# Optimization experiments

Measured on AMD Instinct MI355X. Metric: run time of the kernel, lower is better.

## Reference

```python
import jax, jax.numpy as jnp
import numpy as np
import math

DIM = 4096
N_HEADS = 32
HEAD_DIM = DIM // N_HEADS  # 128
SEQLEN = 2048


def setup_inputs() -> dict:
    key = jax.random.key(0)
    ks = jax.random.split(key, 8)
    x = jax.random.normal(ks[0], (1, SEQLEN, DIM), dtype=jnp.float32)
    # freqs_cis as real view: (seqlen, head_dim//2, 2) = (cos, sin) of rotary angles
    theta = 10000.0 ** (-jnp.arange(0, HEAD_DIM, 2, dtype=jnp.float32) / HEAD_DIM)
    angles = jnp.arange(SEQLEN, dtype=jnp.float32)[:, None] * theta[None, :]
    freqs = jnp.stack([jnp.cos(angles), jnp.sin(angles)], axis=-1)  # (S, 64, 2)
    # causal additive mask (use -1e9 instead of -inf for numeric safety)
    mask = jnp.triu(jnp.full((SEQLEN, SEQLEN), -1e9, dtype=jnp.float32), k=1)[None, None]
    scale = 1.0 / math.sqrt(DIM)
    wq = jax.random.normal(ks[1], (DIM, DIM), dtype=jnp.float32) * scale
    wk = jax.random.normal(ks[2], (DIM, DIM), dtype=jnp.float32) * scale
    wv = jax.random.normal(ks[3], (DIM, DIM), dtype=jnp.float32) * scale
    wo = jax.random.normal(ks[4], (DIM, DIM), dtype=jnp.float32) * scale
    return {"x": x, "start_pos": 0, "freqs": freqs, "mask": mask,
            "wq": wq, "wk": wk, "wv": wv, "wo": wo}


def _rotary(xq, xk, freqs, seqlen, n_heads, head_dim):
    # Faithful to source: note the repo's slice(0, 2) means xq_ == xq (no pair swap).
    ll = freqs[:, :, 0:1]  # (S, hd/2, 1) cos
    rr = freqs[:, :, 1:2]  # (S, hd/2, 1) sin
    fl = jnp.concatenate([ll, ll], axis=-1).reshape(seqlen, 1, head_dim)
    fr = jnp.concatenate([-rr, rr], axis=-1).reshape(seqlen, 1, head_dim)
    xq_ = xq.reshape(seqlen, n_heads, head_dim // 2, 2).reshape(seqlen, n_heads, head_dim)  # == xq
    xk_ = xk.reshape(seqlen, n_heads, head_dim // 2, 2).reshape(seqlen, n_heads, head_dim)  # == xk
    return xq * fl + xq_ * fr, xk * fl + xk_ * fr


def reference(x, start_pos, freqs, mask, wq, wk, wv, wo):
    bsz, seqlen, dim = x.shape  # bsz == 1 (source squeezes batch)
    xs = x[0]  # (S, D) -- HE encrypt/linear/decrypt roundtrip == plain linear
    xq = xs @ wq.T
    xk = xs @ wk.T
    xv = xs @ wv.T
    xq = xq.reshape(seqlen, N_HEADS, HEAD_DIM)
    xk = xk.reshape(seqlen, N_HEADS, HEAD_DIM)
    xv = xv.reshape(seqlen, N_HEADS, HEAD_DIM)
    xq, xk = _rotary(xq, xk, freqs, seqlen, N_HEADS, HEAD_DIM)
    # start_pos == 0 and zero-initialized cache => keys/values are just xk/xv
    q = jnp.transpose(xq, (1, 0, 2))  # (H, S, Dh)
    k = jnp.transpose(xk, (1, 0, 2))
    v = jnp.transpose(xv, (1, 0, 2))
    scores = jnp.einsum('hqd,hkd->hqk', q, k) / math.sqrt(HEAD_DIM)  # (H, S, S)
    scores = scores[None] + mask  # (1, H, S, S)
    probs = jax.nn.softmax(scores, axis=-1)
    out = jnp.einsum('bhqk,hkd->bhqd', probs, v)  # (1, H, S, Dh)
    out = jnp.transpose(out, (0, 2, 1, 3)).reshape(bsz, seqlen, dim)
    return out @ wo.T
```

## Files before the change

kernel.cpp:

```cpp
#include <hip/hip_runtime.h>

#define DIM 4096
#define SEQ 2048
#define NH 32
#define HD 128

typedef __bf16 bf16x8 __attribute__((ext_vector_type(8)));
typedef float f32x4 __attribute__((ext_vector_type(4)));

#define QSCALE 0.12751649736765598f

__device__ inline ushort f2bf(float f) {
    union { float f; unsigned u; } v; v.f = f;
    unsigned r = v.u + 0x7fffu + ((v.u >> 16) & 1u);
    return (ushort)(r >> 16);
}

__global__ void conv_all(const float* __restrict__ x,  const float* __restrict__ wq,
                         const float* __restrict__ wk, const float* __restrict__ wv,
                         const float* __restrict__ wo,
                         ushort* __restrict__ xb,  ushort* __restrict__ wqb,
                         ushort* __restrict__ wkb, ushort* __restrict__ wvb,
                         ushort* __restrict__ wob) {
    int i = blockIdx.x * 256 + threadIdx.x;
    const float* src; ushort* dst; int off;
    const int n4x = (SEQ * DIM) / 4;
    if (i < n4x) { src = x; dst = xb; off = i; }
    else {
        int j = i - n4x;
        int w = j >> 22;
        off = j & ((1 << 22) - 1);
        src = (w == 0) ? wq : (w == 1) ? wk : (w == 2) ? wv : wo;
        dst = (w == 0) ? wqb : (w == 1) ? wkb : (w == 2) ? wvb : wob;
    }
    float4 v = ((const float4*)src)[off];
    ushort4 o;
    o.x = f2bf(v.x); o.y = f2bf(v.y); o.z = f2bf(v.z); o.w = f2bf(v.w);
    ((ushort4*)dst)[off] = o;
}

__global__ __launch_bounds__(256)
void gemm_qkv(const ushort* __restrict__ A,
              const ushort* __restrict__ Bq, const ushort* __restrict__ Bk,
              const ushort* __restrict__ Bv,
              ushort* __restrict__ qout, ushort* __restrict__ kout,
              ushort* __restrict__ vt, const float* __restrict__ freqs) {
    __shared__ __align__(16) ushort sA[128 * 32];
    __shared__ __align__(16) ushort sB[128 * 32];
    const int tid = threadIdx.x;
    const int wave = tid >> 6, lane = tid & 63;
    const int quad = lane >> 4, c = lane & 15;
    const int n0g = blockIdx.x * 128;
    const int wsel = n0g >> 12;
    const int nloc = n0g & 4095;
    const int m0 = blockIdx.y * 128;
    const int wm = (wave >> 1) * 64, wn = (wave & 1) * 64;
    const ushort* B = (wsel == 0) ? Bq : (wsel == 1) ? Bk : Bv;
    const int K = DIM;

    const f32x4 vzero = {0.f, 0.f, 0.f, 0.f};
    f32x4 acc[4][4];
#pragma unroll
    for (int i = 0; i < 4; i++)
#pragma unroll
        for (int j = 0; j < 4; j++) acc[i][j] = vzero;

    const int srow = lane >> 2;
    const int scol = (lane & 3) * 8;
    const size_t arow0 = (size_t)(m0 + wave * 32) * K;
    const size_t brow0 = (size_t)(nloc + wave * 32) * K;

    for (int k0 = 0; k0 < K; k0 += 32) {
#pragma unroll
        for (int j = 0; j < 2; j++) {
            __builtin_amdgcn_global_load_lds(
                (const __attribute__((address_space(1))) void*)(A + arow0 + (size_t)(j * 16 + srow) * K + k0 + scol),
                (__attribute__((address_space(3))) void*)(&sA[(wave * 32 + j * 16) * 32]), 16, 0, 0);
            __builtin_amdgcn_global_load_lds(
                (const __attribute__((address_space(1))) void*)(B + brow0 + (size_t)(j * 16 + srow) * K + k0 + scol),
                (__attribute__((address_space(3))) void*)(&sB[(wave * 32 + j * 16) * 32]), 16, 0, 0);
        }
        __syncthreads();
        bf16x8 af[4], bfr[4];
#pragma unroll
        for (int t = 0; t < 4; t++) {
            af[t]  = *(const bf16x8*)&sA[(wm + t * 16 + c) * 32 + quad * 8];
            bfr[t] = *(const bf16x8*)&sB[(wn + t * 16 + c) * 32 + quad * 8];
        }
#pragma unroll
        for (int mt = 0; mt < 4; mt++)
#pragma unroll
            for (int nt = 0; nt < 4; nt++)
                acc[mt][nt] = __builtin_amdgcn_mfma_f32_16x16x32_bf16(af[mt], bfr[nt], acc[mt][nt], 0, 0, 0);
        __syncthreads();
    }

    if (wsel < 2) {
        ushort* Cw = wsel ? kout : qout;
        const float qs = wsel ? 1.0f : QSCALE;
#pragma unroll
        for (int mt = 0; mt < 4; mt++) {
#pragma unroll
            for (int nt = 0; nt < 4; nt++) {
                int colg = nloc + wn + nt * 16 + c;
                int dh = (colg & 127) >> 1;
#pragma unroll
                for (int r = 0; r < 4; r++) {
                    int row = m0 + wm + mt * 16 + quad * 4 + r;
                    float2 f2 = ((const float2*)freqs)[row * 64 + dh];
                    float f = (f2.x + ((c & 1) ? f2.y : -f2.y)) * qs;
                    Cw[(size_t)row * DIM + colg] = f2bf(acc[mt][nt][r] * f);
                }
            }
        }
    } else {
#pragma unroll
        for (int mt = 0; mt < 4; mt++) {
#pragma unroll
            for (int nt = 0; nt < 4; nt++) {
                int cv = nloc + wn + nt * 16 + c;
                int row0 = m0 + wm + mt * 16 + quad * 4;
                ushort4 o;
                o.x = f2bf(acc[mt][nt][0]); o.y = f2bf(acc[mt][nt][1]);
                o.z = f2bf(acc[mt][nt][2]); o.w = f2bf(acc[mt][nt][3]);
                *(ushort4*)&vt[(size_t)cv * SEQ + row0] = o;
            }
        }
    }
}

__global__ __launch_bounds__(256)
void gemm_f32out(const ushort* __restrict__ A, const ushort* __restrict__ B,
                 float* __restrict__ C, int M, int N, int K) {
    __shared__ __align__(16) ushort sA[128 * 32];
    __shared__ __align__(16) ushort sB[128 * 32];
    const int tid = threadIdx.x;
    const int wave = tid >> 6, lane = tid & 63;
    const int quad = lane >> 4, c = lane & 15;
    const int m0 = blockIdx.y * 128, n0 = blockIdx.x * 128;
    const int wm = (wave >> 1) * 64, wn = (wave & 1) * 64;

    const f32x4 vzero = {0.f, 0.f, 0.f, 0.f};
    f32x4 acc[4][4];
#pragma unroll
    for (int i = 0; i < 4; i++)
#pragma unroll
        for (int j = 0; j < 4; j++) acc[i][j] = vzero;

    const int srow = lane >> 2;
    const int scol = (lane & 3) * 8;
    const size_t arow0 = (size_t)(m0 + wave * 32) * K;
    const size_t brow0 = (size_t)(n0 + wave * 32) * K;

    for (int k0 = 0; k0 < K; k0 += 32) {
#pragma unroll
        for (int j = 0; j < 2; j++) {
            __builtin_amdgcn_global_load_lds(
                (const __attribute__((address_space(1))) void*)(A + arow0 + (size_t)(j * 16 + srow) * K + k0 + scol),
                (__attribute__((address_space(3))) void*)(&sA[(wave * 32 + j * 16) * 32]), 16, 0, 0);
            __builtin_amdgcn_global_load_lds(
                (const __attribute__((address_space(1))) void*)(B + brow0 + (size_t)(j * 16 + srow) * K + k0 + scol),
                (__attribute__((address_space(3))) void*)(&sB[(wave * 32 + j * 16) * 32]), 16, 0, 0);
        }
        __syncthreads();
        bf16x8 af[4], bfr[4];
#pragma unroll
        for (int t = 0; t < 4; t++) {
            af[t]  = *(const bf16x8*)&sA[(wm + t * 16 + c) * 32 + quad * 8];
            bfr[t] = *(const bf16x8*)&sB[(wn + t * 16 + c) * 32 + quad * 8];
        }
#pragma unroll
        for (int mt = 0; mt < 4; mt++)
#pragma unroll
            for (int nt = 0; nt < 4; nt++)
                acc[mt][nt] = __builtin_amdgcn_mfma_f32_16x16x32_bf16(af[mt], bfr[nt], acc[mt][nt], 0, 0, 0);
        __syncthreads();
    }

#pragma unroll
    for (int mt = 0; mt < 4; mt++)
#pragma unroll
        for (int nt = 0; nt < 4; nt++)
#pragma unroll
            for (int r = 0; r < 4; r++) {
                int row = m0 + wm + mt * 16 + quad * 4 + r;
                int col = n0 + wn + nt * 16 + c;
                C[(size_t)row * N + col] = acc[mt][nt][r];
            }
}

__global__ __launch_bounds__(256)
void flash_kernel(const ushort* __restrict__ Q, const ushort* __restrict__ K,
                  const ushort* __restrict__ Vt, ushort* __restrict__ O) {
    const int bi = blockIdx.x;
    const int h = bi & (NH - 1);
    const int p = bi >> 5;
    __shared__ __align__(16) ushort sK[64 * 128];
    __shared__ __align__(16) ushort sVt[128 * 64];
    __shared__ __align__(16) ushort sP[4][16 * 72];
    const int tid = threadIdx.x, wave = tid >> 6, lane = tid & 63;
    const int quad = lane >> 4, c = lane & 15;

    for (int pass = 0; pass < 2; pass++) {
        const int qb = pass ? (SEQ / 64 - 1 - p) : p;
        const int q0 = qb * 64;

        bf16x8 qf[4];
        {
            const ushort* Qp = Q + (size_t)(q0 + wave * 16 + c) * DIM + h * HD;
#pragma unroll
            for (int ks = 0; ks < 4; ks++) qf[ks] = *(const bf16x8*)(Qp + ks * 32 + quad * 8);
        }
        const f32x4 vzero = {0.f, 0.f, 0.f, 0.f};
        f32x4 oa[8];
#pragma unroll
        for (int dt = 0; dt < 8; dt++) oa[dt] = vzero;
        float ms[4], ls[4];
#pragma unroll
        for (int r = 0; r < 4; r++) { ms[r] = -1e30f; ls[r] = 0.f; }

        for (int kt = 0; kt <= qb; kt++) {
            __syncthreads();
#pragma unroll
            for (int i = 0; i < 4; i++) {
                int lr = wave * 16 + i * 4 + (lane >> 4);
                int ch = lane & 15;
                int g = (ch & 8) | ((ch ^ lr) & 7);
                __builtin_amdgcn_global_load_lds(
                    (const __attribute__((address_space(1))) void*)(K + (size_t)(kt * 64 + lr) * DIM + h * HD + g * 8),
                    (__attribute__((address_space(3))) void*)(&sK[(wave * 16 + i * 4) * 128]), 16, 0, 0);
            }
#pragma unroll
            for (int i = 0; i < 4; i++) {
                int ld = wave * 32 + i * 8 + (lane >> 3);
                int ch = lane & 7;
                int g = (ch ^ ld) & 7;
                __builtin_amdgcn_global_load_lds(
                    (const __attribute__((address_space(1))) void*)(Vt + (size_t)(h * HD + ld) * SEQ + kt * 64 + g * 8),
                    (__attribute__((address_space(3))) void*)(&sVt[(wave * 32 + i * 8) * 64]), 16, 0, 0);
            }
            __syncthreads();

            f32x4 s[4];
#pragma unroll
            for (int nt = 0; nt < 4; nt++) s[nt] = vzero;
#pragma unroll
            for (int ks = 0; ks < 4; ks++)
#pragma unroll
                for (int nt = 0; nt < 4; nt++) {
                    int lr = nt * 16 + c;
                    int gc = ks * 4 + quad;
                    int pch = (gc & 8) | ((gc ^ lr) & 7);
                    bf16x8 kf = *(const bf16x8*)&sK[lr * 128 + pch * 8];
                    s[nt] = __builtin_amdgcn_mfma_f32_16x16x32_bf16(qf[ks], kf, s[nt], 0, 0, 0);
                }

            if (kt == qb) {
#pragma unroll
                for (int nt = 0; nt < 4; nt++)
#pragma unroll
                    for (int r = 0; r < 4; r++) {
                        int keyg = nt * 16 + c;
                        int qg   = wave * 16 + quad * 4 + r;
                        if (keyg > qg) s[nt][r] = -1e30f;
                    }
            }

            float mnew[4], alpha[4];
#pragma unroll
            for (int r = 0; r < 4; r++) {
                float v = fmaxf(fmaxf(s[0][r], s[1][r]), fmaxf(s[2][r], s[3][r]));
                v = fmaxf(v, __shfl_xor(v, 1));
                v = fmaxf(v, __shfl_xor(v, 2));
                v = fmaxf(v, __shfl_xor(v, 4));
                v = fmaxf(v, __shfl_xor(v, 8));
                mnew[r]  = fmaxf(ms[r], v);
                alpha[r] = exp2f(ms[r] - mnew[r]);
                ms[r]    = mnew[r];
            }
            float rs[4] = {0.f, 0.f, 0.f, 0.f};
#pragma unroll
            for (int nt = 0; nt < 4; nt++)
#pragma unroll
                for (int r = 0; r < 4; r++) {
                    float pv = exp2f(s[nt][r] - mnew[r]);
                    rs[r] += pv;
                    sP[wave][(quad * 4 + r) * 72 + nt * 16 + c] = f2bf(pv);
                }
#pragma unroll
            for (int r = 0; r < 4; r++) {
                float v = rs[r];
                v += __shfl_xor(v, 1);
                v += __shfl_xor(v, 2);
                v += __shfl_xor(v, 4);
                v += __shfl_xor(v, 8);
                ls[r] = ls[r] * alpha[r] + v;
            }
#pragma unroll
            for (int dt = 0; dt < 8; dt++)
#pragma unroll
                for (int r = 0; r < 4; r++) oa[dt][r] *= alpha[r];

            __asm__ volatile("s_waitcnt lgkmcnt(0)" ::: "memory");

#pragma unroll
            for (int k2 = 0; k2 < 2; k2++) {
                bf16x8 pf = *(const bf16x8*)&sP[wave][c * 72 + k2 * 32 + quad * 8];
#pragma unroll
                for (int dt = 0; dt < 8; dt++) {
                    int ld = dt * 16 + c;
                    int gc = k2 * 4 + quad;
                    int pch = (gc ^ ld) & 7;
                    bf16x8 vf = *(const bf16x8*)&sVt[ld * 64 + pch * 8];
                    oa[dt] = __builtin_amdgcn_mfma_f32_16x16x32_bf16(pf, vf, oa[dt], 0, 0, 0);
                }
            }
        }

#pragma unroll
        for (int r = 0; r < 4; r++) {
            float inv = 1.f / ls[r];
            int row = q0 + wave * 16 + quad * 4 + r;
#pragma unroll
            for (int dt = 0; dt < 8; dt++)
                O[(size_t)row * DIM + h * HD + dt * 16 + c] = f2bf(oa[dt][r] * inv);
        }
    }
}

extern "C" void kernel_launch(void* const* d_in, const int* in_sizes, int n_in,
                              void* d_out, int out_size, void* d_ws, size_t ws_size,
                              hipStream_t stream) {
    const float* x     = (const float*)d_in[0];
    const float* freqs = (const float*)d_in[2];
    const float* wq    = (const float*)d_in[4];
    const float* wk    = (const float*)d_in[5];
    const float* wv    = (const float*)d_in[6];
    const float* wo    = (const float*)d_in[7];
    float* out = (float*)d_out;

    ushort* xb    = (ushort*)d_ws;
    ushort* wqb   = xb    + (size_t)SEQ * DIM;
    ushort* wkb   = wqb   + (size_t)DIM * DIM;
    ushort* wvb   = wkb   + (size_t)DIM * DIM;
    ushort* wob   = wvb   + (size_t)DIM * DIM;
    ushort* qbuf  = wob   + (size_t)DIM * DIM;
    ushort* kbuf  = qbuf  + (size_t)SEQ * DIM;
    ushort* vtbuf = kbuf  + (size_t)SEQ * DIM;
    ushort* obuf  = vtbuf + (size_t)SEQ * DIM;

    const int n4tot = (SEQ * DIM + 4 * DIM * DIM) / 4;
    conv_all<<<n4tot / 256, 256, 0, stream>>>(x, wq, wk, wv, wo, xb, wqb, wkb, wvb, wob);

    gemm_qkv<<<dim3(3 * DIM / 128, SEQ / 128), 256, 0, stream>>>(
        xb, wqb, wkb, wvb, qbuf, kbuf, vtbuf, freqs);

    flash_kernel<<<dim3(NH * SEQ / 128), 256, 0, stream>>>(qbuf, kbuf, vtbuf, obuf);

    gemm_f32out<<<dim3(DIM / 128, SEQ / 128), 256, 0, stream>>>(obuf, wob, out, SEQ, DIM, DIM);
}
```

Before: 812.1 us.

## Swizzle LDS tile layout and remap GEMM block order for cache locality

Both bf16 GEMM kernels now rotate the 16-byte column groups within each LDS row based on the row index, both when writing with global_load_lds and when reading fragments, to reduce LDS bank conflicts. The 2D grid is flattened to 1D and block indices are remapped so consecutive blocks cover paired M tiles while sharing N tiles, aiming at better L2 reuse across XCDs. This adds index arithmetic, and a mismatch between the write and read swizzles would corrupt results.

```diff
diff --git a/kernel.cpp b/kernel.cpp
--- a/kernel.cpp
+++ b/kernel.cpp
@@ -47,13 +47,16 @@
               ushort* __restrict__ vt, const float* __restrict__ freqs) {
     __shared__ __align__(16) ushort sA[128 * 32];
     __shared__ __align__(16) ushort sB[128 * 32];
+    const int bi = blockIdx.x;
+    const int jj = bi >> 3;
+    const int mblk = (bi & 7) * 2 + (jj & 1);
+    const int nblk = jj >> 1;
+    const int wsel = nblk >> 5;
+    const int nloc = (nblk & 31) * 128;
+    const int m0 = mblk * 128;
     const int tid = threadIdx.x;
     const int wave = tid >> 6, lane = tid & 63;
     const int quad = lane >> 4, c = lane & 15;
-    const int n0g = blockIdx.x * 128;
-    const int wsel = n0g >> 12;
-    const int nloc = n0g & 4095;
-    const int m0 = blockIdx.y * 128;
     const int wm = (wave >> 1) * 64, wn = (wave & 1) * 64;
     const ushort* B = (wsel == 0) ? Bq : (wsel == 1) ? Bk : Bv;
     const int K = DIM;
@@ -66,7 +69,9 @@
         for (int j = 0; j < 4; j++) acc[i][j] = vzero;
 
     const int srow = lane >> 2;
-    const int scol = (lane & 3) * 8;
+    const int sg   = ((lane & 3) - (srow >> 1)) & 3;
+    const int scol = sg * 8;
+    const int rpos = (quad + ((c >> 1) & 3)) & 3;
     const size_t arow0 = (size_t)(m0 + wave * 32) * K;
     const size_t brow0 = (size_t)(nloc + wave * 32) * K;
 
@@ -84,8 +89,8 @@
         bf16x8 af[4], bfr[4];
 #pragma unroll
         for (int t = 0; t < 4; t++) {
-            af[t]  = *(const bf16x8*)&sA[(wm + t * 16 + c) * 32 + quad * 8];
-            bfr[t] = *(const bf16x8*)&sB[(wn + t * 16 + c) * 32 + quad * 8];
+            af[t]  = *(const bf16x8*)&sA[(wm + t * 16 + c) * 32 + rpos * 8];
+            bfr[t] = *(const bf16x8*)&sB[(wn + t * 16 + c) * 32 + rpos * 8];
         }
 #pragma unroll
         for (int mt = 0; mt < 4; mt++)
@@ -134,10 +139,14 @@
                  float* __restrict__ C, int M, int N, int K) {
     __shared__ __align__(16) ushort sA[128 * 32];
     __shared__ __align__(16) ushort sB[128 * 32];
+    const int bi = blockIdx.x;
+    const int jj = bi >> 3;
+    const int mblk = (bi & 7) * 2 + (jj & 1);
+    const int nblk = jj >> 1;
+    const int m0 = mblk * 128, n0 = nblk * 128;
     const int tid = threadIdx.x;
     const int wave = tid >> 6, lane = tid & 63;
     const int quad = lane >> 4, c = lane & 15;
-    const int m0 = blockIdx.y * 128, n0 = blockIdx.x * 128;
     const int wm = (wave >> 1) * 64, wn = (wave & 1) * 64;
 
     const f32x4 vzero = {0.f, 0.f, 0.f, 0.f};
@@ -148,7 +157,9 @@
         for (int j = 0; j < 4; j++) acc[i][j] = vzero;
 
     const int srow = lane >> 2;
-    const int scol = (lane & 3) * 8;
+    const int sg   = ((lane & 3) - (srow >> 1)) & 3;
+    const int scol = sg * 8;
+    const int rpos = (quad + ((c >> 1) & 3)) & 3;
     const size_t arow0 = (size_t)(m0 + wave * 32) * K;
     const size_t brow0 = (size_t)(n0 + wave * 32) * K;
 
@@ -166,8 +177,8 @@
         bf16x8 af[4], bfr[4];
 #pragma unroll
         for (int t = 0; t < 4; t++) {
-            af[t]  = *(const bf16x8*)&sA[(wm + t * 16 + c) * 32 + quad * 8];
-            bfr[t] = *(const bf16x8*)&sB[(wn + t * 16 + c) * 32 + quad * 8];
+            af[t]  = *(const bf16x8*)&sA[(wm + t * 16 + c) * 32 + rpos * 8];
+            bfr[t] = *(const bf16x8*)&sB[(wn + t * 16 + c) * 32 + rpos * 8];
         }
 #pragma unroll
         for (int mt = 0; mt < 4; mt++)
@@ -352,10 +363,10 @@
     const int n4tot = (SEQ * DIM + 4 * DIM * DIM) / 4;
     conv_all<<<n4tot / 256, 256, 0, stream>>>(x, wq, wk, wv, wo, xb, wqb, wkb, wvb, wob);
 
-    gemm_qkv<<<dim3(3 * DIM / 128, SEQ / 128), 256, 0, stream>>>(
+    gemm_qkv<<<dim3(3 * DIM / 128 * SEQ / 128), 256, 0, stream>>>(
         xb, wqb, wkb, wvb, qbuf, kbuf, vtbuf, freqs);
 
     flash_kernel<<<dim3(NH * SEQ / 128), 256, 0, stream>>>(qbuf, kbuf, vtbuf, obuf);
 
-    gemm_f32out<<<dim3(DIM / 128, SEQ / 128), 256, 0, stream>>>(obuf, wob, out, SEQ, DIM, DIM);
-}
+    gemm_f32out<<<dim3(DIM / 128 * SEQ / 128), 256, 0, stream>>>(obuf, wob, out, SEQ, DIM, DIM);
+}
```

Result: no change. 804.8 us (-0.9%).
